# Kernel optimization log

Hardware: AMD Instinct MI355X
Metric: run time of the kernel (lower is better)

Reference implementation:

```python
import jax, jax.numpy as jnp
import numpy as np

B, T, D, A = 8, 256, 512, 512  # hidden dim D must equal attn size A per the TF code


def setup_inputs() -> dict:
    key = jax.random.key(0)
    ks = jax.random.split(key, 12)
    g = lambda k, shp, fan: jax.random.normal(k, shp, jnp.float32) * (1.0 / np.sqrt(fan))
    return {
        "state_outputs": jax.random.normal(ks[0], (B, T, D), jnp.float32),
        "final_state": jax.random.normal(ks[1], (B, D), jnp.float32),
        "intent_v": g(ks[2], (A,), A),
        "W_ih": g(ks[3], (D, A), D), "b_ih": jnp.zeros((A,), jnp.float32),
        "W_ii": g(ks[4], (D, A), D), "b_ii": jnp.zeros((A,), jnp.float32),
        "slot_v": g(ks[5], (A,), A),
        "W_sh": g(ks[6], (D, A), D), "b_sh": jnp.zeros((A,), jnp.float32),
        "W_si": g(ks[7], (D, A), D), "b_si": jnp.zeros((A,), jnp.float32),
    }


def reference(state_outputs, final_state, intent_v, W_ih, b_ih, W_ii, b_ii,
              slot_v, W_sh, b_sh, W_si, b_si):
    # ---- intent attention ----
    ih = jnp.einsum('btd,da->bta', state_outputs, W_ih) + b_ih        # [B,T,A]
    ii = final_state @ W_ii + b_ii                                     # [B,A]
    intent_score = jnp.sum(intent_v * jnp.tanh(ih + ii[:, None, :]), axis=-1)  # [B,T]
    intent_w = jax.nn.softmax(intent_score, axis=-1)
    c_intent = jnp.einsum('bt,btd->bd', intent_w, state_outputs)       # [B,D]

    # ---- slot attention ----
    sh = jnp.einsum('btd,da->bta', state_outputs, W_sh) + b_sh         # keys   [B,T,A]
    si = jnp.einsum('btd,da->bta', state_outputs, W_si) + b_si         # queries[B,T,A]
    # score[b,t,s] over pairs: tanh(sh[b,s] + si[b,t]) . slot_v
    slot_score = jnp.sum(slot_v * jnp.tanh(sh[:, None, :, :] + si[:, :, None, :]), axis=-1)  # [B,T,T]
    slot_w = jax.nn.softmax(slot_score, axis=-1)
    c_slot = jnp.einsum('bts,bsd->btd', slot_w, state_outputs)         # [B,T,D]
    return c_slot, c_intent
```

## Files before the change

### kernel.cpp

```cpp
#include <hip/hip_runtime.h>

#define BB 8
#define TT 256
#define DD 512
#define AA 512

#define PS 2.8853900817779268f
#define LOG2E 1.4426950408889634f

typedef __attribute__((ext_vector_type(8))) short short8;
typedef __attribute__((ext_vector_type(4))) float f32x4;

__device__ __forceinline__ float fast_tanh(float x) {
    float e = __builtin_amdgcn_exp2f(x * PS);
    float r = __builtin_amdgcn_rcpf(1.0f + e);
    return fmaf(-2.0f, r, 1.0f);
}

__device__ __forceinline__ ushort f2bf(float x) {
    uint u = __float_as_uint(x);
    uint r = (u + 0x7fffu + ((u >> 16) & 1u)) >> 16;
    return (ushort)r;
}
__device__ __forceinline__ float bf2f(ushort h) {
    return __uint_as_float(((uint)h) << 16);
}

__global__ __launch_bounds__(256) void prep(const float* __restrict__ SO,
                                            ushort* __restrict__ Ast,
                                            const float* __restrict__ Wsh,
                                            const float* __restrict__ Wsi,
                                            const float* __restrict__ Wih,
                                            ushort* __restrict__ Wt,
                                            const float* __restrict__ fs_g,
                                            const float* __restrict__ Wii,
                                            const float* __restrict__ bii,
                                            float* __restrict__ ii) {
    const int bid = blockIdx.x;
    const int tid = threadIdx.x;
    __shared__ float T[32][33];
    __shared__ float fs[DD];

    if (bid < 16) {
        int b = bid >> 1, half = bid & 1;
        int a = half * 256 + tid;
        fs[tid]       = fs_g[b * DD + tid];
        fs[tid + 256] = fs_g[b * DD + tid + 256];
        __syncthreads();
        float acc = bii[a];
        #pragma unroll 8
        for (int d = 0; d < DD; ++d)
            acc = fmaf(fs[d], Wii[(size_t)d * AA + a], acc);
        ii[b * AA + a] = acc;
    } else if (bid < 784) {
        int lbid = bid - 16;
        int z = lbid >> 8;
        int rem = lbid & 255;
        const float* W = (z == 0) ? Wsh : (z == 1) ? Wsi : Wih;
        int k0 = (rem & 15) * 32, n0 = (rem >> 4) * 32;
        int tx = tid & 31, ty = tid >> 5;
        #pragma unroll
        for (int r = 0; r < 4; ++r) {
            int kl = ty * 4 + r;
            T[kl][tx] = W[(size_t)(k0 + kl) * 512 + n0 + tx];
        }
        __syncthreads();
        size_t nbase = (size_t)z * 512 + n0;
        #pragma unroll
        for (int r = 0; r < 4; ++r) {
            int nl = ty * 4 + r;
            float v = T[tx][nl];
            ushort hi = f2bf(v);
            ushort lo = f2bf(v - bf2f(hi));
            Wt[(nbase + nl) * 1024 + k0 + tx]       = hi;
            Wt[(nbase + nl) * 1024 + 512 + k0 + tx] = lo;
        }
    } else {
        int qid = (bid - 784) * 256 + tid;
        int m = qid >> 7;
        int k4 = (qid & 127) * 4;
        float4 v = *reinterpret_cast<const float4*>(&SO[(size_t)m * 512 + k4]);
        ushort4 hi, lo;
        hi.x = f2bf(v.x); lo.x = f2bf(v.x - bf2f(hi.x));
        hi.y = f2bf(v.y); lo.y = f2bf(v.y - bf2f(hi.y));
        hi.z = f2bf(v.z); lo.z = f2bf(v.z - bf2f(hi.z));
        hi.w = f2bf(v.w); lo.w = f2bf(v.w - bf2f(hi.w));
        *reinterpret_cast<ushort4*>(&Ast[(size_t)m * 1024 + k4])       = hi;
        *reinterpret_cast<ushort4*>(&Ast[(size_t)m * 1024 + 512 + k4]) = lo;
    }
}

__global__ __launch_bounds__(256) void gemm_mfma(
    const ushort* __restrict__ Ast, const ushort* __restrict__ Wt,
    const float* __restrict__ bsh, const float* __restrict__ bsi,
    const float* __restrict__ bih,
    const float* __restrict__ ii, const float* __restrict__ iv,
    float* __restrict__ EhT, float* __restrict__ Es, float* __restrict__ ipart) {
    __shared__ __align__(16) ushort Al[2][128 * 32];
    __shared__ __align__(16) ushort Bl[2][128 * 32];
    const int tid = threadIdx.x;
    const int wave = tid >> 6, lane = tid & 63;
    const int wr = wave >> 1, wc = wave & 1;
    const int m0 = blockIdx.x * 128;
    const int by = blockIdx.y;
    const int l15 = lane & 15, kb = lane >> 4;

    f32x4 acc[4][4] = {};

    const char* Ab = reinterpret_cast<const char*>(Ast);
    const char* Bb = reinterpret_cast<const char*>(Wt);
    char* AlB = reinterpret_cast<char*>(&Al[0][0]);
    char* BlB = reinterpret_cast<char*>(&Bl[0][0]);

    const int srow  = tid >> 1;
    const int sslot = (tid & 1) * 2;
    const int swz   = (srow >> 1) & 3;
    const int lw0 = srow * 64 + ((sslot    ) ^ swz) * 16;
    const int lw1 = srow * 64 + ((sslot + 1) ^ swz) * 16;
    const char* agp = Ab + (size_t)(m0 + srow) * 2048 + sslot * 16;
    const char* bgp = Bb + (size_t)(by * 128 + srow) * 2048 + sslot * 16;

    int aro[4], bro[4];
    #pragma unroll
    for (int i = 0; i < 4; ++i) {
        int ra = wr * 64 + i * 16 + l15;
        aro[i] = ra * 64 + ((kb ^ ((ra >> 1) & 3)) * 16);
        int rb = wc * 64 + i * 16 + l15;
        bro[i] = rb * 64 + ((kb ^ ((rb >> 1) & 3)) * 16);
    }

    #define ABYTE(k0) (((k0) < 1024 ? (k0) : (k0) - 1024) * 2)
    #define BBYTE(k0) (((k0) < 512 ? (k0) : (k0) - 512) * 2)

    {
        short8 a0 = *reinterpret_cast<const short8*>(agp + ABYTE(0));
        short8 a1 = *reinterpret_cast<const short8*>(agp + ABYTE(0) + 16);
        short8 b0 = *reinterpret_cast<const short8*>(bgp + BBYTE(0));
        short8 b1 = *reinterpret_cast<const short8*>(bgp + BBYTE(0) + 16);
        *reinterpret_cast<short8*>(AlB + lw0) = a0;
        *reinterpret_cast<short8*>(AlB + lw1) = a1;
        *reinterpret_cast<short8*>(BlB + lw0) = b0;
        *reinterpret_cast<short8*>(BlB + lw1) = b1;
    }
    __syncthreads();

    int cur = 0;
    for (int it = 0; it < 48; ++it) {
        short8 a0, a1, b0, b1;
        const bool pf = (it + 1 < 48);
        if (pf) {
            int k0 = (it + 1) * 32;
            int ab = ABYTE(k0), bb = BBYTE(k0);
            a0 = *reinterpret_cast<const short8*>(agp + ab);
            a1 = *reinterpret_cast<const short8*>(agp + ab + 16);
            b0 = *reinterpret_cast<const short8*>(bgp + bb);
            b1 = *reinterpret_cast<const short8*>(bgp + bb + 16);
        }
        const char* Ac = AlB + cur * 8192;
        const char* Bc = BlB + cur * 8192;
        short8 af[4], bf[4];
        #pragma unroll
        for (int i = 0; i < 4; ++i) {
            af[i] = *reinterpret_cast<const short8*>(Ac + aro[i]);
            bf[i] = *reinterpret_cast<const short8*>(Bc + bro[i]);
        }
        #pragma unroll
        for (int i = 0; i < 4; ++i)
            #pragma unroll
            for (int j = 0; j < 4; ++j)
                acc[i][j] = __builtin_amdgcn_mfma_f32_16x16x32_bf16(
                    af[i], bf[j], acc[i][j], 0, 0, 0);
        if (pf) {
            char* An = AlB + (cur ^ 1) * 8192;
            char* Bn = BlB + (cur ^ 1) * 8192;
            *reinterpret_cast<short8*>(An + lw0) = a0;
            *reinterpret_cast<short8*>(An + lw1) = a1;
            *reinterpret_cast<short8*>(Bn + lw0) = b0;
            *reinterpret_cast<short8*>(Bn + lw1) = b1;
        }
        __syncthreads();
        cur ^= 1;
    }

    const int b = m0 >> 8;
    const int region = by >> 2;
    if (region == 0) {
        #pragma unroll
        for (int i = 0; i < 4; ++i) {
            int t0 = (m0 & 255) + wr * 64 + i * 16 + kb * 4;
            #pragma unroll
            for (int j = 0; j < 4; ++j) {
                int n = by * 128 + wc * 64 + j * 16 + l15;
                float bbv = bsh[n];
                float4 v;
                v.x = __builtin_amdgcn_exp2f((acc[i][j][0] + bbv) * PS);
                v.y = __builtin_amdgcn_exp2f((acc[i][j][1] + bbv) * PS);
                v.z = __builtin_amdgcn_exp2f((acc[i][j][2] + bbv) * PS);
                v.w = __builtin_amdgcn_exp2f((acc[i][j][3] + bbv) * PS);
                *reinterpret_cast<float4*>(&EhT[((size_t)b * 512 + n) * 256 + t0]) = v;
            }
        }
    } else if (region == 1) {
        #pragma unroll
        for (int i = 0; i < 4; ++i) {
            #pragma unroll
            for (int j = 0; j < 4; ++j) {
                int n = (by - 4) * 128 + wc * 64 + j * 16 + l15;
                float bbv = bsi[n];
                #pragma unroll
                for (int r = 0; r < 4; ++r) {
                    int m = m0 + wr * 64 + i * 16 + kb * 4 + r;
                    Es[(size_t)m * 512 + n] = __builtin_amdgcn_exp2f((acc[i][j][r] + bbv) * PS);
                }
            }
        }
    } else {
        int slot = (by - 8) * 2 + wc;
        #pragma unroll
        for (int i = 0; i < 4; ++i) {
            float p0 = 0.f, p1 = 0.f, p2 = 0.f, p3 = 0.f;
            #pragma unroll
            for (int j = 0; j < 4; ++j) {
                int n = (by - 8) * 128 + wc * 64 + j * 16 + l15;
                float add = bih[n] + ii[b * 512 + n];
                float w = iv[n];
                p0 = fmaf(w, fast_tanh(acc[i][j][0] + add), p0);
                p1 = fmaf(w, fast_tanh(acc[i][j][1] + add), p1);
                p2 = fmaf(w, fast_tanh(acc[i][j][2] + add), p2);
                p3 = fmaf(w, fast_tanh(acc[i][j][3] + add), p3);
            }
            #pragma unroll
            for (int off = 1; off < 16; off <<= 1) {
                p0 += __shfl_xor(p0, off);
                p1 += __shfl_xor(p1, off);
                p2 += __shfl_xor(p2, off);
                p3 += __shfl_xor(p3, off);
            }
            int mb = m0 + wr * 64 + i * 16 + kb * 4;
            if (l15 == 0) ipart[slot * 2048 + mb + 0] = p0;
            if (l15 == 1) ipart[slot * 2048 + mb + 1] = p1;
            if (l15 == 2) ipart[slot * 2048 + mb + 2] = p2;
            if (l15 == 3) ipart[slot * 2048 + mb + 3] = p3;
        }
    }
}

#define TS 64
#define KS 16
#define LPAD 72

__global__ __launch_bounds__(256) void k0_ii(const float* __restrict__ fs_g,
                                             const float* __restrict__ Wii,
                                             const float* __restrict__ bii,
                                             float* __restrict__ ii) {
    int b = blockIdx.x, tid = threadIdx.x;
    int a = blockIdx.y * 256 + tid;
    __shared__ float fs[DD];
    fs[tid]       = fs_g[b * DD + tid];
    fs[tid + 256] = fs_g[b * DD + tid + 256];
    __syncthreads();
    float acc = bii[a];
    #pragma unroll 8
    for (int d = 0; d < DD; ++d)
        acc = fmaf(fs[d], Wii[(size_t)d * AA + a], acc);
    ii[b * AA + a] = acc;
}

__global__ __launch_bounds__(256) void k1_gemm_old(
    const float* __restrict__ SO,
    const float* __restrict__ Wsh, const float* __restrict__ bsh,
    const float* __restrict__ Wsi, const float* __restrict__ bsi,
    const float* __restrict__ Wih, const float* __restrict__ bih,
    const float* __restrict__ ii, const float* __restrict__ iv,
    float* __restrict__ EhT, float* __restrict__ Es, float* __restrict__ ipart) {
    const int mode = blockIdx.z;
    const float* W;
    const float* bias;
    if (mode == 0)      { W = Wsh; bias = bsh; }
    else if (mode == 1) { W = Wsi; bias = bsi; }
    else                { W = Wih; bias = bih; }

    const int m0 = blockIdx.x * TS;
    const int n0 = blockIdx.y * TS;
    const int tid = threadIdx.x;
    const int tx = tid & 15, ty = tid >> 4;

    __shared__ __align__(16) float As[KS][LPAD];
    __shared__ __align__(16) float Bs[KS][LPAD];
    __shared__ __align__(16) float Cs[TS][LPAD];

    float acc[4][4] = {};
    const int arow = tid >> 2;
    const int akc  = (tid & 3) * 4;
    const int brw  = tid >> 4;
    const int bnc  = (tid & 15) * 4;

    for (int k0 = 0; k0 < DD; k0 += KS) {
        float4 av = *reinterpret_cast<const float4*>(&SO[(m0 + arow) * DD + k0 + akc]);
        As[akc + 0][arow] = av.x;
        As[akc + 1][arow] = av.y;
        As[akc + 2][arow] = av.z;
        As[akc + 3][arow] = av.w;
        float4 bv = *reinterpret_cast<const float4*>(&W[(k0 + brw) * AA + n0 + bnc]);
        *reinterpret_cast<float4*>(&Bs[brw][bnc]) = bv;
        __syncthreads();
        #pragma unroll
        for (int kk = 0; kk < KS; ++kk) {
            float4 a4 = *reinterpret_cast<const float4*>(&As[kk][ty * 4]);
            float4 b4 = *reinterpret_cast<const float4*>(&Bs[kk][tx * 4]);
            float av_[4] = {a4.x, a4.y, a4.z, a4.w};
            float bv_[4] = {b4.x, b4.y, b4.z, b4.w};
            #pragma unroll
            for (int i = 0; i < 4; ++i)
                #pragma unroll
                for (int j = 0; j < 4; ++j)
                    acc[i][j] = fmaf(av_[i], bv_[j], acc[i][j]);
        }
        __syncthreads();
    }

    if (mode == 1) {
        #pragma unroll
        for (int i = 0; i < 4; ++i) {
            int m = m0 + ty * 4 + i;
            float4 v;
            v.x = __builtin_amdgcn_exp2f((acc[i][0] + bias[n0 + tx * 4 + 0]) * PS);
            v.y = __builtin_amdgcn_exp2f((acc[i][1] + bias[n0 + tx * 4 + 1]) * PS);
            v.z = __builtin_amdgcn_exp2f((acc[i][2] + bias[n0 + tx * 4 + 2]) * PS);
            v.w = __builtin_amdgcn_exp2f((acc[i][3] + bias[n0 + tx * 4 + 3]) * PS);
            *reinterpret_cast<float4*>(&Es[(size_t)m * AA + n0 + tx * 4]) = v;
        }
    } else if (mode == 0) {
        #pragma unroll
        for (int i = 0; i < 4; ++i)
            #pragma unroll
            for (int j = 0; j < 4; ++j)
                Cs[tx * 4 + j][ty * 4 + i] =
                    __builtin_amdgcn_exp2f((acc[i][j] + bias[n0 + tx * 4 + j]) * PS);
        __syncthreads();
        int row = tid >> 2, part = tid & 3;
        int bb = m0 >> 8;
        int tstart = (m0 & 255) + part * 16;
        float* dst = &EhT[bb * (AA * TT) + (n0 + row) * TT + tstart];
        #pragma unroll
        for (int q = 0; q < 4; ++q) {
            float4 v = *reinterpret_cast<const float4*>(&Cs[row][part * 16 + q * 4]);
            *reinterpret_cast<float4*>(&dst[q * 4]) = v;
        }
    } else {
        int bb = m0 >> 8;
        #pragma unroll
        for (int i = 0; i < 4; ++i) {
            float p = 0.f;
            #pragma unroll
            for (int j = 0; j < 4; ++j) {
                int n = n0 + tx * 4 + j;
                float x = acc[i][j] + bias[n] + ii[bb * AA + n];
                p = fmaf(iv[n], fast_tanh(x), p);
            }
            Cs[ty * 4 + i][tx] = p;
        }
        __syncthreads();
        if (tid < 64) {
            float s = 0.f;
            #pragma unroll
            for (int k = 0; k < 16; ++k) s += Cs[tid][k];
            ipart[blockIdx.y * 2048 + m0 + tid] = s;
        }
    }
}

__global__ __launch_bounds__(512) void k3_fused(const float* __restrict__ SO,
                                                const float* __restrict__ EhT,
                                                const float* __restrict__ Es,
                                                const float* __restrict__ sv_g,
                                                const float* __restrict__ ipart,
                                                float* __restrict__ out_cslot,
                                                float* __restrict__ out_cint) {
    const int bid = blockIdx.x;
    const int tid = threadIdx.x;

    __shared__ __align__(8) float est[512][2];
    __shared__ float sv[512];
    __shared__ float yp[2][2][256];
    __shared__ __align__(8) float wlt[256][2];
    __shared__ float redm[2][4];
    __shared__ float reds[2][4];
    __shared__ float redI[256];
    __shared__ float wlI[256];

    if (bid >= 8) {
        const int sb_ = bid - 8;
        const int b = sb_ & 7;
        const int t0 = (sb_ >> 3) * 2;
        const int s = tid & 255, ah = tid >> 8;

        {
            const float* esrc = &Es[(size_t)(b * 256 + t0) * 512];
            int i0 = tid;
            est[i0 & 511][i0 >> 9] = esrc[i0];
            int i1 = tid + 512;
            est[i1 & 511][i1 >> 9] = esrc[i1];
            sv[tid] = sv_g[tid];
        }
        __syncthreads();

        const int abase = ah * 256;
        const float* hp = &EhT[((size_t)b * 512 + abase) * 256 + s];
        float y0 = 0.f, y1 = 0.f;
        for (int a0 = 0; a0 < 256; a0 += 8) {
            float h[8];
            #pragma unroll
            for (int u = 0; u < 8; ++u) h[u] = hp[(a0 + u) * 256];
            #pragma unroll
            for (int u = 0; u < 8; ++u) {
                int a = abase + a0 + u;
                float2 e2 = *reinterpret_cast<const float2*>(&est[a][0]);
                float v = sv[a];
                float x0 = fmaf(h[u], e2.x, 1.0f);
                y0 = fmaf(v, __builtin_amdgcn_rcpf(x0), y0);
                float x1 = fmaf(h[u], e2.y, 1.0f);
                y1 = fmaf(v, __builtin_amdgcn_rcpf(x1), y1);
            }
        }
        yp[ah][0][s] = y0; yp[ah][1][s] = y1;
        __syncthreads();

        const int q = ah;
        const int wg = (tid >> 6) & 3;
        float y = yp[0][q][s] + yp[1][q][s];
        float mn = y;
        #pragma unroll
        for (int off = 1; off < 64; off <<= 1)
            mn = fminf(mn, __shfl_xor(mn, off));
        if ((tid & 63) == 0) redm[q][wg] = mn;
        __syncthreads();
        mn = fminf(fminf(redm[q][0], redm[q][1]), fminf(redm[q][2], redm[q][3]));
        float e = __builtin_amdgcn_exp2f(PS * (mn - y));
        float sm = e;
        #pragma unroll
        for (int off = 1; off < 64; off <<= 1)
            sm += __shfl_xor(sm, off);
        if ((tid & 63) == 0) reds[q][wg] = sm;
        __syncthreads();
        sm = (reds[q][0] + reds[q][1]) + (reds[q][2] + reds[q][3]);
        wlt[s][q] = e * __builtin_amdgcn_rcpf(sm);
        __syncthreads();

        const int d = tid;
        const float* sop = &SO[(size_t)b * 256 * 512 + d];
        float c0 = 0.f, c1 = 0.f;
        for (int s0 = 0; s0 < 256; s0 += 4) {
            float so[4];
            #pragma unroll
            for (int u = 0; u < 4; ++u) so[u] = sop[(s0 + u) * 512];
            #pragma unroll
            for (int u = 0; u < 4; ++u) {
                float2 w2 = *reinterpret_cast<const float2*>(&wlt[s0 + u][0]);
                c0 = fmaf(w2.x, so[u], c0);
                c1 = fmaf(w2.y, so[u], c1);
            }
        }
        float* op = &out_cslot[((size_t)(b * 256 + t0)) * 512 + d];
        op[0] = c0; op[512] = c1;
    } else {
        const int b = bid;
        float sc = 0.f;
        if (tid < 256) {
            #pragma unroll
            for (int nb = 0; nb < 8; ++nb) sc += ipart[nb * 2048 + b * 256 + tid];
            redI[tid] = sc;
        }
        __syncthreads();
        for (int off = 128; off > 0; off >>= 1) {
            if (tid < off) redI[tid] = fmaxf(redI[tid], redI[tid + off]);
            __syncthreads();
        }
        float mx = redI[0];
        __syncthreads();
        float e = 0.f;
        if (tid < 256) { e = __builtin_amdgcn_exp2f((sc - mx) * LOG2E); redI[tid] = e; }
        __syncthreads();
        for (int off = 128; off > 0; off >>= 1) {
            if (tid < off) redI[tid] += redI[tid + off];
            __syncthreads();
        }
        if (tid < 256) wlI[tid] = e * __builtin_amdgcn_rcpf(redI[0]);
        __syncthreads();
        const int d = tid;
        float c = 0.f;
        const float* sop = &SO[(size_t)b * 256 * 512 + d];
        for (int s0 = 0; s0 < 256; s0 += 4) {
            float so[4];
            #pragma unroll
            for (int u = 0; u < 4; ++u) so[u] = sop[(s0 + u) * 512];
            #pragma unroll
            for (int u = 0; u < 4; ++u) c = fmaf(wlI[s0 + u], so[u], c);
        }
        out_cint[(size_t)b * 512 + d] = c;
    }
}

extern "C" void kernel_launch(void* const* d_in, const int* in_sizes, int n_in,
                              void* d_out, int out_size, void* d_ws, size_t ws_size,
                              hipStream_t stream) {
    const float* SO  = (const float*)d_in[0];
    const float* FS  = (const float*)d_in[1];
    const float* IV  = (const float*)d_in[2];
    const float* Wih = (const float*)d_in[3];
    const float* bih = (const float*)d_in[4];
    const float* Wii = (const float*)d_in[5];
    const float* bii = (const float*)d_in[6];
    const float* SV  = (const float*)d_in[7];
    const float* Wsh = (const float*)d_in[8];
    const float* bsh = (const float*)d_in[9];
    const float* Wsi = (const float*)d_in[10];
    const float* bsi = (const float*)d_in[11];

    float* ws    = (float*)d_ws;
    float* EhT   = ws;
    float* Es    = ws + 1048576;
    float* ii    = ws + 2097152;
    float* ipart = ws + 2101248;
    ushort* Ast  = (ushort*)(ws + 2134016);
    ushort* Wt   = (ushort*)(ws + 3182592);
    const size_t NEED = (size_t)3969024 * 4;

    float* out_cslot = (float*)d_out;
    float* out_cint  = out_cslot + BB * TT * DD;

    if (ws_size >= NEED) {
        prep<<<1808, 256, 0, stream>>>(SO, Ast, Wsh, Wsi, Wih, Wt, FS, Wii, bii, ii);
        gemm_mfma<<<dim3(16, 12), 256, 0, stream>>>(Ast, Wt, bsh, bsi, bih, ii, IV,
                                                    EhT, Es, ipart);
        k3_fused<<<1032, 512, 0, stream>>>(SO, EhT, Es, SV, ipart, out_cslot, out_cint);
    } else {
        k0_ii<<<dim3(BB, 2), 256, 0, stream>>>(FS, Wii, bii, ii);
        k1_gemm_old<<<dim3(32, 8, 3), 256, 0, stream>>>(SO, Wsh, bsh, Wsi, bsi, Wih, bih,
                                                        ii, IV, EhT, Es, ipart);
        k3_fused<<<1032, 512, 0, stream>>>(SO, EhT, Es, SV, ipart, out_cslot, out_cint);
    }
}
```

Before: 113.3 us.

## Process four query rows per block with 2x4 register tile in slot attention

The fused slot-attention kernel now handles four query rows per block instead of two. Each thread computes a 2-key by 4-query register tile, so every EhT load and every weighted SO load feeds more arithmetic, and the grid halves to 520 blocks. The cost is more registers and shared memory per block and fewer blocks to fill the GPU. The number of intent partials also becomes a runtime argument.

Result: faster. 104.5 us (-7.8%).

```diff
diff --git a/kernel.cpp b/kernel.cpp
--- a/kernel.cpp
+++ b/kernel.cpp
@@ -376,99 +376,114 @@
                                                 const float* __restrict__ sv_g,
                                                 const float* __restrict__ ipart,
                                                 float* __restrict__ out_cslot,
-                                                float* __restrict__ out_cint) {
+                                                float* __restrict__ out_cint,
+                                                int npart) {
     const int bid = blockIdx.x;
     const int tid = threadIdx.x;
 
-    __shared__ __align__(8) float est[512][2];
-    __shared__ float sv[512];
-    __shared__ float yp[2][2][256];
-    __shared__ __align__(8) float wlt[256][2];
-    __shared__ float redm[2][4];
-    __shared__ float reds[2][4];
+    __shared__ __align__(16) float est[512][4];
+    __shared__ __align__(16) float sv[512];
+    __shared__ __align__(8)  float yp[4][4][256];
+    __shared__ __align__(16) float wlt[256][4];
+    __shared__ float redm[4][2];
+    __shared__ float reds[4][2];
     __shared__ float redI[256];
     __shared__ float wlI[256];
 
     if (bid >= 8) {
         const int sb_ = bid - 8;
         const int b = sb_ & 7;
-        const int t0 = (sb_ >> 3) * 2;
-        const int s = tid & 255, ah = tid >> 8;
+        const int t0 = (sb_ >> 3) * 4;
+        const int sp = tid & 127;
+        const int ah = tid >> 7;
+        const int abase = ah * 128;
 
         {
             const float* esrc = &Es[(size_t)(b * 256 + t0) * 512];
-            int i0 = tid;
-            est[i0 & 511][i0 >> 9] = esrc[i0];
-            int i1 = tid + 512;
-            est[i1 & 511][i1 >> 9] = esrc[i1];
+            #pragma unroll
+            for (int i = tid; i < 2048; i += 512) est[i & 511][i >> 9] = esrc[i];
             sv[tid] = sv_g[tid];
         }
         __syncthreads();
 
-        const int abase = ah * 256;
-        const float* hp = &EhT[((size_t)b * 512 + abase) * 256 + s];
-        float y0 = 0.f, y1 = 0.f;
-        for (int a0 = 0; a0 < 256; a0 += 8) {
-            float h[8];
-            #pragma unroll
-            for (int u = 0; u < 8; ++u) h[u] = hp[(a0 + u) * 256];
-            #pragma unroll
-            for (int u = 0; u < 8; ++u) {
-                int a = abase + a0 + u;
-                float2 e2 = *reinterpret_cast<const float2*>(&est[a][0]);
-                float v = sv[a];
-                float x0 = fmaf(h[u], e2.x, 1.0f);
-                y0 = fmaf(v, __builtin_amdgcn_rcpf(x0), y0);
-                float x1 = fmaf(h[u], e2.y, 1.0f);
-                y1 = fmaf(v, __builtin_amdgcn_rcpf(x1), y1);
-            }
-        }
-        yp[ah][0][s] = y0; yp[ah][1][s] = y1;
-        __syncthreads();
-
-        const int q = ah;
-        const int wg = (tid >> 6) & 3;
-        float y = yp[0][q][s] + yp[1][q][s];
-        float mn = y;
+        const float* hp = &EhT[((size_t)b * 512 + abase) * 256 + 2 * sp];
+        float a00=0.f,a01=0.f,a10=0.f,a11=0.f,a20=0.f,a21=0.f,a30=0.f,a31=0.f;
+        for (int a0 = 0; a0 < 128; a0 += 4) {
+            float4 v4 = *reinterpret_cast<const float4*>(&sv[abase + a0]);
+            float2 h[4];
+            #pragma unroll
+            for (int u = 0; u < 4; ++u)
+                h[u] = *reinterpret_cast<const float2*>(&hp[(a0 + u) * 256]);
+            #pragma unroll
+            for (int u = 0; u < 4; ++u) {
+                float4 e4 = *reinterpret_cast<const float4*>(&est[abase + a0 + u][0]);
+                float vv = (u == 0) ? v4.x : (u == 1) ? v4.y : (u == 2) ? v4.z : v4.w;
+                float hx = h[u].x, hy = h[u].y;
+                a00 = fmaf(vv, __builtin_amdgcn_rcpf(fmaf(hx, e4.x, 1.f)), a00);
+                a01 = fmaf(vv, __builtin_amdgcn_rcpf(fmaf(hy, e4.x, 1.f)), a01);
+                a10 = fmaf(vv, __builtin_amdgcn_rcpf(fmaf(hx, e4.y, 1.f)), a10);
+                a11 = fmaf(vv, __builtin_amdgcn_rcpf(fmaf(hy, e4.y, 1.f)), a11);
+                a20 = fmaf(vv, __builtin_amdgcn_rcpf(fmaf(hx, e4.z, 1.f)), a20);
+                a21 = fmaf(vv, __builtin_amdgcn_rcpf(fmaf(hy, e4.z, 1.f)), a21);
+                a30 = fmaf(vv, __builtin_amdgcn_rcpf(fmaf(hx, e4.w, 1.f)), a30);
+                a31 = fmaf(vv, __builtin_amdgcn_rcpf(fmaf(hy, e4.w, 1.f)), a31);
+            }
+        }
+        *reinterpret_cast<float2*>(&yp[ah][0][2 * sp]) = make_float2(a00, a01);
+        *reinterpret_cast<float2*>(&yp[ah][1][2 * sp]) = make_float2(a10, a11);
+        *reinterpret_cast<float2*>(&yp[ah][2][2 * sp]) = make_float2(a20, a21);
+        *reinterpret_cast<float2*>(&yp[ah][3][2 * sp]) = make_float2(a30, a31);
+        __syncthreads();
+
+        const int g = ah;
+        const int L = sp;
+        const int w2 = (tid >> 6) & 1;
+        float yL = (yp[0][g][L]       + yp[1][g][L])       + (yp[2][g][L]       + yp[3][g][L]);
+        float yH = (yp[0][g][L + 128] + yp[1][g][L + 128]) + (yp[2][g][L + 128] + yp[3][g][L + 128]);
+        float mn = fminf(yL, yH);
         #pragma unroll
         for (int off = 1; off < 64; off <<= 1)
             mn = fminf(mn, __shfl_xor(mn, off));
-        if ((tid & 63) == 0) redm[q][wg] = mn;
-        __syncthreads();
-        mn = fminf(fminf(redm[q][0], redm[q][1]), fminf(redm[q][2], redm[q][3]));
-        float e = __builtin_amdgcn_exp2f(PS * (mn - y));
-        float sm = e;
+        if ((tid & 63) == 0) redm[g][w2] = mn;
+        __syncthreads();
+        mn = fminf(redm[g][0], redm[g][1]);
+        float eL = __builtin_amdgcn_exp2f(PS * (mn - yL));
+        float eH = __builtin_amdgcn_exp2f(PS * (mn - yH));
+        float sm = eL + eH;
         #pragma unroll
         for (int off = 1; off < 64; off <<= 1)
             sm += __shfl_xor(sm, off);
-        if ((tid & 63) == 0) reds[q][wg] = sm;
-        __syncthreads();
-        sm = (reds[q][0] + reds[q][1]) + (reds[q][2] + reds[q][3]);
-        wlt[s][q] = e * __builtin_amdgcn_rcpf(sm);
+        if ((tid & 63) == 0) reds[g][w2] = sm;
+        __syncthreads();
+        sm = reds[g][0] + reds[g][1];
+        float rs = __builtin_amdgcn_rcpf(sm);
+        wlt[L][g]       = eL * rs;
+        wlt[L + 128][g] = eH * rs;
         __syncthreads();
 
         const int d = tid;
         const float* sop = &SO[(size_t)b * 256 * 512 + d];
-        float c0 = 0.f, c1 = 0.f;
+        float c0 = 0.f, c1 = 0.f, c2 = 0.f, c3 = 0.f;
         for (int s0 = 0; s0 < 256; s0 += 4) {
             float so[4];
             #pragma unroll
             for (int u = 0; u < 4; ++u) so[u] = sop[(s0 + u) * 512];
             #pragma unroll
             for (int u = 0; u < 4; ++u) {
-                float2 w2 = *reinterpret_cast<const float2*>(&wlt[s0 + u][0]);
-                c0 = fmaf(w2.x, so[u], c0);
-                c1 = fmaf(w2.y, so[u], c1);
+                float4 w4 = *reinterpret_cast<const float4*>(&wlt[s0 + u][0]);
+                c0 = fmaf(w4.x, so[u], c0);
+                c1 = fmaf(w4.y, so[u], c1);
+                c2 = fmaf(w4.z, so[u], c2);
+                c3 = fmaf(w4.w, so[u], c3);
             }
         }
         float* op = &out_cslot[((size_t)(b * 256 + t0)) * 512 + d];
-        op[0] = c0; op[512] = c1;
+        op[0] = c0; op[512] = c1; op[1024] = c2; op[1536] = c3;
     } else {
         const int b = bid;
         float sc = 0.f;
         if (tid < 256) {
-            #pragma unroll
-            for (int nb = 0; nb < 8; ++nb) sc += ipart[nb * 2048 + b * 256 + tid];
+            for (int nb = 0; nb < npart; ++nb) sc += ipart[nb * 2048 + b * 256 + tid];
             redI[tid] = sc;
         }
         __syncthreads();
@@ -533,11 +548,11 @@
         prep<<<1808, 256, 0, stream>>>(SO, Ast, Wsh, Wsi, Wih, Wt, FS, Wii, bii, ii);
         gemm_mfma<<<dim3(16, 12), 256, 0, stream>>>(Ast, Wt, bsh, bsi, bih, ii, IV,
                                                     EhT, Es, ipart);
-        k3_fused<<<1032, 512, 0, stream>>>(SO, EhT, Es, SV, ipart, out_cslot, out_cint);
+        k3_fused<<<520, 512, 0, stream>>>(SO, EhT, Es, SV, ipart, out_cslot, out_cint, 8);
     } else {
         k0_ii<<<dim3(BB, 2), 256, 0, stream>>>(FS, Wii, bii, ii);
         k1_gemm_old<<<dim3(32, 8, 3), 256, 0, stream>>>(SO, Wsh, bsh, Wsi, bsi, Wih, bih,
                                                         ii, IV, EhT, Es, ipart);
-        k3_fused<<<1032, 512, 0, stream>>>(SO, EhT, Es, SV, ipart, out_cslot, out_cint);
-    }
-}
+        k3_fused<<<520, 512, 0, stream>>>(SO, EhT, Es, SV, ipart, out_cslot, out_cint, 8);
+    }
+}
```
